# Kernel tuning notes

Hardware: AMD Instinct MI355X
Metric: run time of the kernel (lower is better)

Reference implementation:

```python
import jax, jax.numpy as jnp
import numpy as np

B, N, M, F_DIM, H, D = 4, 2048, 2048, 512, 8, 64  # M == num_time
MID = H * D
EPS = 1e-5


def _layernorm(x, w, b):
    mu = jnp.mean(x, axis=-1, keepdims=True)
    var = jnp.var(x, axis=-1, keepdims=True)
    return (x - mu) * jax.lax.rsqrt(var + EPS) * w + b


def setup_inputs() -> dict:
    key = jax.random.key(0)
    ks = jax.random.split(key, 12)
    s = 0.02
    return {
        "x": jax.random.normal(ks[0], (B, N, F_DIM), jnp.float32),
        "context": jax.random.normal(ks[1], (B, M, F_DIM), jnp.float32),
        "pos_emb": jax.random.normal(ks[2], (M, F_DIM), jnp.float32) * s,  # nn.Embedding(num_time, features)
        "ln_w": jnp.ones((F_DIM,), jnp.float32),
        "ln_b": jnp.zeros((F_DIM,), jnp.float32),
        "lnc_w": jnp.ones((F_DIM,), jnp.float32),
        "lnc_b": jnp.zeros((F_DIM,), jnp.float32),
        "Wq": jax.random.normal(ks[3], (F_DIM, MID), jnp.float32) * s,
        "Wk": jax.random.normal(ks[4], (F_DIM, MID), jnp.float32) * s,
        "Wv": jax.random.normal(ks[5], (F_DIM, MID), jnp.float32) * s,
        "Wout": jax.random.normal(ks[6], (MID, F_DIM), jnp.float32) * s,
        "bout": jnp.zeros((F_DIM,), jnp.float32),
    }


def reference(x, context, pos_emb, ln_w, ln_b, lnc_w, lnc_b, Wq, Wk, Wv, Wout, bout):
    scale = D ** (-0.5)
    keys = jnp.broadcast_to(pos_emb[None], (x.shape[0], M, F_DIM))  # [B, T, F]
    xn = _layernorm(x, ln_w, ln_b)
    kn = _layernorm(keys, ln_w, ln_b)          # same norm as x (self.norm)
    cn = _layernorm(context, lnc_w, lnc_b)
    q = (xn @ Wq).reshape(x.shape[0], N, H, D).transpose(0, 2, 1, 3)  # b h n d
    k = (kn @ Wk).reshape(x.shape[0], M, H, D).transpose(0, 2, 1, 3)  # b h m d
    v = (cn @ Wv).reshape(x.shape[0], M, H, D).transpose(0, 2, 1, 3)  # b h m d
    sim = jnp.einsum('bhnd,bhmd->bhnm', q, k) * scale
    attn = jax.nn.softmax(sim, axis=-1)
    out = jnp.einsum('bhnm,bhmd->bhnd', attn, v)
    out = out.transpose(0, 2, 1, 3).reshape(x.shape[0], N, MID)  # b n (h d)
    return out @ Wout + bout
```

## Files before the change

### kernel.cpp

```cpp
#include <hip/hip_runtime.h>
#include <stdint.h>

#define B_ 4
#define N_ 2048
#define M_ 2048
#define F_ 512
#define H_ 8
#define D_ 64

typedef __bf16 bf16x8 __attribute__((ext_vector_type(8)));
typedef float f32x4 __attribute__((ext_vector_type(4)));
typedef float f32x16 __attribute__((ext_vector_type(16)));

typedef const __attribute__((address_space(1))) uint32_t* gas_ptr;
typedef __attribute__((address_space(3))) uint32_t* las_ptr;

__device__ inline ushort f32_bf16(float f) {
    union { float f; uint32_t u; } v; v.f = f;
    uint32_t r = v.u + 0x7FFFu + ((v.u >> 16) & 1u);
    return (ushort)(r >> 16);
}

__global__ __launch_bounds__(128) void prep_kernel(
    const float* __restrict__ x, const float* __restrict__ ctx, const float* __restrict__ pos,
    const float* __restrict__ lnw, const float* __restrict__ lnb,
    const float* __restrict__ lncw, const float* __restrict__ lncb,
    const float* __restrict__ Wq, const float* __restrict__ Wk,
    const float* __restrict__ Wv, const float* __restrict__ Wo,
    ushort* __restrict__ xn, ushort* __restrict__ kn, ushort* __restrict__ cn,
    ushort* __restrict__ WqT, ushort* __restrict__ WkT,
    ushort* __restrict__ WvT, ushort* __restrict__ WoT)
{
    __shared__ float red[4];
    __shared__ float tile[32][33];
    int r = blockIdx.x;
    int tid = threadIdx.x;

    if (r < B_ * N_ + M_ + B_ * M_) {
        const float* src; ushort* dst; const float* w; const float* bp;
        if (r < B_ * N_) {
            src = x + (size_t)r * F_; dst = xn + (size_t)r * F_; w = lnw; bp = lnb;
        } else if (r < B_ * N_ + M_) {
            int rr = r - B_ * N_;
            src = pos + (size_t)rr * F_; dst = kn + (size_t)rr * F_; w = lnw; bp = lnb;
        } else {
            int rr = r - (B_ * N_ + M_);
            src = ctx + (size_t)rr * F_; dst = cn + (size_t)rr * F_; w = lncw; bp = lncb;
        }
        int wave = tid >> 6, lane = tid & 63;
        float4 v = reinterpret_cast<const float4*>(src)[tid];
        float s = v.x + v.y + v.z + v.w;
        float sq = v.x * v.x + v.y * v.y + v.z * v.z + v.w * v.w;
        #pragma unroll
        for (int mask = 1; mask < 64; mask <<= 1) {
            s += __shfl_xor(s, mask, 64);
            sq += __shfl_xor(sq, mask, 64);
        }
        if (lane == 0) { red[wave * 2] = s; red[wave * 2 + 1] = sq; }
        __syncthreads();
        float S = red[0] + red[2], SQ = red[1] + red[3];
        float mean = S * (1.0f / F_);
        float var = SQ * (1.0f / F_) - mean * mean;
        float rstd = rsqrtf(var + 1e-5f);
        float4 wv = reinterpret_cast<const float4*>(w)[tid];
        float4 bv = reinterpret_cast<const float4*>(bp)[tid];
        ushort4 o;
        o.x = f32_bf16((v.x - mean) * rstd * wv.x + bv.x);
        o.y = f32_bf16((v.y - mean) * rstd * wv.y + bv.y);
        o.z = f32_bf16((v.z - mean) * rstd * wv.z + bv.z);
        o.w = f32_bf16((v.w - mean) * rstd * wv.w + bv.w);
        reinterpret_cast<ushort4*>(dst)[tid] = o;
        return;
    }

    int wblk = r - (B_ * N_ + M_ + B_ * M_);
    const float* W; ushort* WT;
    switch (wblk >> 8) {
        case 0: W = Wq; WT = WqT; break;
        case 1: W = Wk; WT = WkT; break;
        case 2: W = Wv; WT = WvT; break;
        default: W = Wo; WT = WoT; break;
    }
    int ti = wblk & 255;
    int n0 = (ti & 15) * 32, k0 = (ti >> 4) * 32;
    int tx = tid & 31, ty = tid >> 5;
    #pragma unroll
    for (int j = 0; j < 8; ++j)
        tile[ty + j * 4][tx] = W[(size_t)(k0 + ty + j * 4) * F_ + n0 + tx];
    __syncthreads();
    #pragma unroll
    for (int j = 0; j < 8; ++j)
        WT[(size_t)(n0 + ty + j * 4) * F_ + k0 + tx] = f32_bf16(tile[tx][ty + j * 4]);
}

__device__ __forceinline__ void gemm_body(
    const ushort* __restrict__ A, const ushort* __restrict__ BT,
    const float* __restrict__ bias, void* __restrict__ Cout,
    int mode, int bx, int by)
{
    __shared__ ushort As[128][64];
    __shared__ ushort Bs[128][64];
    int tid = threadIdx.x;
    int row0 = by * 128, col0 = bx * 128;
    int wv = tid >> 6, lane = tid & 63;
    int wm = wv >> 1, wn = wv & 1;
    f32x4 acc[4][4] = {};

    const int lrow8 = lane >> 3;
    const int chs = ((lane & 7) ^ (lrow8 & 7)) * 8;
    const ushort* agp = A + (size_t)(row0 + wv * 32 + lrow8) * F_ + chs;
    const ushort* bgp = BT + (size_t)(col0 + wv * 32 + lrow8) * F_ + chs;

    for (int k0 = 0; k0 < F_; k0 += 64) {
        #pragma unroll
        for (int j = 0; j < 4; ++j) {
            __builtin_amdgcn_global_load_lds(
                (gas_ptr)(const void*)(agp + k0 + j * 8 * F_),
                (las_ptr)(void*)&As[wv * 32 + j * 8][0], 16, 0, 0);
            __builtin_amdgcn_global_load_lds(
                (gas_ptr)(const void*)(bgp + k0 + j * 8 * F_),
                (las_ptr)(void*)&Bs[wv * 32 + j * 8][0], 16, 0, 0);
        }
        __syncthreads();
        #pragma unroll
        for (int kt = 0; kt < 2; ++kt) {
            int lrow = lane & 15;
            int ch = ((kt * 4 + (lane >> 4)) ^ (lane & 7)) * 8;
            bf16x8 af[4], bfr[4];
            #pragma unroll
            for (int mt = 0; mt < 4; ++mt)
                af[mt] = *reinterpret_cast<const bf16x8*>(&As[wm * 64 + mt * 16 + lrow][ch]);
            #pragma unroll
            for (int nt = 0; nt < 4; ++nt)
                bfr[nt] = *reinterpret_cast<const bf16x8*>(&Bs[wn * 64 + nt * 16 + lrow][ch]);
            #pragma unroll
            for (int mt = 0; mt < 4; ++mt)
                #pragma unroll
                for (int nt = 0; nt < 4; ++nt)
                    acc[mt][nt] = __builtin_amdgcn_mfma_f32_16x16x32_bf16(
                        af[mt], bfr[nt], acc[mt][nt], 0, 0, 0);
        }
        __syncthreads();
    }

    int lr4 = (lane >> 4) * 4, lc = lane & 15;
    #pragma unroll
    for (int mt = 0; mt < 4; ++mt) {
        #pragma unroll
        for (int nt = 0; nt < 4; ++nt) {
            int ccol = col0 + wn * 64 + nt * 16 + lc;
            float bv = (mode == 1) ? bias[ccol] : 0.0f;
            #pragma unroll
            for (int j = 0; j < 4; ++j) {
                int crow = row0 + wm * 64 + mt * 16 + lr4 + j;
                float val = acc[mt][nt][j] + bv;
                if (mode == 1) {
                    reinterpret_cast<float*>(Cout)[(size_t)crow * F_ + ccol] = val;
                } else if (mode == 0) {
                    reinterpret_cast<ushort*>(Cout)[(size_t)crow * F_ + ccol] = f32_bf16(val);
                } else if (mode == 2) {
                    int h = ccol >> 6, t = crow >> 7, s = (crow >> 6) & 1;
                    int ab = (crow >> 5) & 1, l31 = crow & 31;
                    int ds = (ccol >> 4) & 3, g2 = (ccol >> 3) & 1, e = ccol & 7;
                    size_t addr = (((size_t)(h * 16 + t) * 16 + s * 8 + ds * 2 + ab) * 64
                                   + g2 * 32 + l31) * 8 + e;
                    reinterpret_cast<ushort*>(Cout)[addr] = f32_bf16(val);
                } else {
                    int b2 = crow >> 11, m = crow & 2047;
                    int h = ccol >> 6, d = ccol & 63;
                    int bh = b2 * 8 + h, hh = d >> 5, l31 = d & 31;
                    int t = m >> 7, s = (m >> 6) & 1, s_ = (m >> 4) & 3;
                    int g2 = (m >> 3) & 1, i = m & 7;
                    size_t addr = (((size_t)(bh * 16 + t) * 16 + hh * 8 + s * 4 + s_) * 64
                                   + g2 * 32 + l31) * 8 + i;
                    reinterpret_cast<ushort*>(Cout)[addr] = f32_bf16(val);
                }
            }
        }
    }
}

__global__ __launch_bounds__(256) void qkv_gemm_kernel(
    const ushort* __restrict__ xn, const ushort* __restrict__ kn,
    const ushort* __restrict__ cn,
    const ushort* __restrict__ WqT, const ushort* __restrict__ WkT,
    const ushort* __restrict__ WvT,
    ushort* __restrict__ qb, ushort* __restrict__ kF, ushort* __restrict__ vF)
{
    int bid = blockIdx.x;
    if (bid < 256) {
        gemm_body(xn, WqT, nullptr, (void*)qb, 0, bid & 3, bid >> 2);
    } else if (bid < 320) {
        int t = bid - 256;
        gemm_body(kn, WkT, nullptr, (void*)kF, 2, t & 3, t >> 2);
    } else {
        int t = bid - 320;
        gemm_body(cn, WvT, nullptr, (void*)vF, 3, t & 3, t >> 2);
    }
}

__global__ __launch_bounds__(256) void out_gemm_kernel(
    const ushort* __restrict__ A, const ushort* __restrict__ WoT,
    const float* __restrict__ bias, float* __restrict__ out)
{
    gemm_body(A, WoT, bias, (void*)out, 1, blockIdx.x & 3, blockIdx.x >> 2);
}

#define MAKE_PA(dst, p, ss) do {                                               \
    uint32_t w0_, w1_, w2_, w3_;                                               \
    asm("v_cvt_pk_bf16_f32 %0, %1, %2" : "=v"(w0_) : "v"(p[8*(ss)+0]), "v"(p[8*(ss)+1])); \
    asm("v_cvt_pk_bf16_f32 %0, %1, %2" : "=v"(w1_) : "v"(p[8*(ss)+2]), "v"(p[8*(ss)+3])); \
    asm("v_cvt_pk_bf16_f32 %0, %1, %2" : "=v"(w2_) : "v"(p[8*(ss)+4]), "v"(p[8*(ss)+5])); \
    asm("v_cvt_pk_bf16_f32 %0, %1, %2" : "=v"(w3_) : "v"(p[8*(ss)+6]), "v"(p[8*(ss)+7])); \
    asm("v_permlane32_swap_b32 %0, %1" : "+v"(w0_), "+v"(w2_));                \
    asm("v_permlane32_swap_b32 %0, %1" : "+v"(w1_), "+v"(w3_));                \
    union { uint32_t w[4]; bf16x8 v; } u_;                                     \
    u_.w[0] = w0_; u_.w[1] = w1_; u_.w[2] = w2_; u_.w[3] = w3_;                \
    dst = u_.v;                                                                \
} while (0)

#define KLOAD(DST, u) do {                                                     \
    const ushort* _p = kfb_ + (size_t)(u) * 4096 + lane * 8;                   \
    _Pragma("unroll")                                                          \
    for (int f_ = 0; f_ < 8; ++f_)                                             \
        DST[f_] = *reinterpret_cast<const bf16x8*>(_p + f_ * 512);             \
} while (0)

#define VLOAD(DST, u) do {                                                     \
    const ushort* _p = vfb_ + (size_t)((u) >> 1) * 8192 +                      \
                       ((u) & 1) * 4 * 512 + lane * 8;                         \
    _Pragma("unroll")                                                          \
    for (int hh_ = 0; hh_ < 2; ++hh_)                                          \
        _Pragma("unroll")                                                      \
        for (int s2_ = 0; s2_ < 4; ++s2_)                                      \
            DST[hh_ * 4 + s2_] = *reinterpret_cast<const bf16x8*>(             \
                _p + (hh_ * 8 + s2_) * 512);                                   \
} while (0)

#define COMPUTE_HALF(QF, OACC, LR, AB) do {                                    \
    f32x16 sS;                                                                 \
    _Pragma("unroll")                                                          \
    for (int j = 0; j < 16; ++j) sS[j] = 0.0f;                                 \
    __builtin_amdgcn_s_setprio(1);                                             \
    _Pragma("unroll")                                                          \
    for (int ds_ = 0; ds_ < 4; ++ds_)                                          \
        sS = __builtin_amdgcn_mfma_f32_32x32x16_bf16(kR[ds_ * 2 + (AB)], QF[ds_], sS, 0, 0, 0); \
    __builtin_amdgcn_s_setprio(0);                                             \
    float pf[16];                                                              \
    _Pragma("unroll")                                                          \
    for (int j = 0; j < 16; ++j)                                               \
        pf[j] = __builtin_amdgcn_exp2f(sS[j] * c1);                            \
    float r0 = 0.0f, r1 = 0.0f, r2 = 0.0f, r3 = 0.0f;                          \
    _Pragma("unroll")                                                          \
    for (int j = 0; j < 16; j += 4) {                                          \
        r0 += pf[j];     r1 += pf[j + 1];                                      \
        r2 += pf[j + 2]; r3 += pf[j + 3];                                      \
    }                                                                          \
    LR += (r0 + r1) + (r2 + r3);                                               \
    bf16x8 pa0, pa1;                                                           \
    MAKE_PA(pa0, pf, 0);                                                       \
    MAKE_PA(pa1, pf, 1);                                                       \
    __builtin_amdgcn_s_setprio(1);                                             \
    _Pragma("unroll")                                                          \
    for (int hh = 0; hh < 2; ++hh) {                                           \
        OACC[hh] = __builtin_amdgcn_mfma_f32_32x32x16_bf16(                    \
            pa0, vR[hh * 4 + (AB) * 2], OACC[hh], 0, 0, 0);                    \
        OACC[hh] = __builtin_amdgcn_mfma_f32_32x32x16_bf16(                    \
            pa1, vR[hh * 4 + (AB) * 2 + 1], OACC[hh], 0, 0, 0);                \
    }                                                                          \
    __builtin_amdgcn_s_setprio(0);                                             \
} while (0)

__global__ __launch_bounds__(512, 1) void attn_kernel(
    const ushort* __restrict__ q,
    const ushort* __restrict__ kF,
    const ushort* __restrict__ vF,
    ushort* __restrict__ o)
{
    const int wave = threadIdx.x >> 6, lane = threadIdx.x & 63;
    const int l31 = lane & 31, g = lane >> 5;
    const int qpair = wave & 3, half = wave >> 2;
    const int bid = blockIdx.x;
    const int qx = bid >> 5, bh = bid & 31;
    const int b = bh >> 3, h = bh & 7;
    const int q0 = qx * 256 + qpair * 64;

    __shared__ float ols[4][64][64];
    __shared__ float lls[4][2][64];

    bf16x8 qfA[4], qfB[4];
    const ushort* qrowA = q + (size_t)(b * N_ + q0 + l31) * F_ + h * 64 + g * 8;
    const ushort* qrowB = qrowA + 32 * F_;
    #pragma unroll
    for (int ds = 0; ds < 4; ++ds) {
        qfA[ds] = *reinterpret_cast<const bf16x8*>(qrowA + ds * 16);
        qfB[ds] = *reinterpret_cast<const bf16x8*>(qrowB + ds * 16);
    }

    float l0 = 0.0f, l1 = 0.0f;
    f32x16 oaccA[2], oaccB[2];
    #pragma unroll
    for (int hh = 0; hh < 2; ++hh)
        #pragma unroll
        for (int j = 0; j < 16; ++j) { oaccA[hh][j] = 0.0f; oaccB[hh][j] = 0.0f; }

    const ushort* kfb_ = kF + (size_t)h * 16 * 16 * 512;
    const ushort* vfb_ = vF + (size_t)bh * 16 * 16 * 512;
    const float c1 = 0.18033688f;

    bf16x8 kR[8], vR[8];
    const int ubase = half * 16;

    #pragma unroll 1
    for (int uu = 0; uu < 16; ++uu) {
        int u = ubase + uu;
        KLOAD(kR, u);
        VLOAD(vR, u);
        COMPUTE_HALF(qfA, oaccA, l0, 0);
        COMPUTE_HALF(qfB, oaccB, l1, 0);
        COMPUTE_HALF(qfA, oaccA, l0, 1);
        COMPUTE_HALF(qfB, oaccB, l1, 1);
    }

    l0 += __shfl_xor(l0, 32, 64);
    l1 += __shfl_xor(l1, 32, 64);

    if (half) {
        #pragma unroll
        for (int hh = 0; hh < 2; ++hh)
            #pragma unroll
            for (int j = 0; j < 16; ++j) {
                ols[qpair][hh * 16 + j][lane] = oaccA[hh][j];
                ols[qpair][32 + hh * 16 + j][lane] = oaccB[hh][j];
            }
        lls[qpair][0][lane] = l0;
        lls[qpair][1][lane] = l1;
    }
    __syncthreads();
    if (!half) {
        #pragma unroll
        for (int hh = 0; hh < 2; ++hh)
            #pragma unroll
            for (int j = 0; j < 16; ++j) {
                oaccA[hh][j] += ols[qpair][hh * 16 + j][lane];
                oaccB[hh][j] += ols[qpair][32 + hh * 16 + j][lane];
            }
        l0 += lls[qpair][0][lane];
        l1 += lls[qpair][1][lane];
        float li0 = 1.0f / l0, li1 = 1.0f / l1;
        float rli0[16], rli1[16];
        #pragma unroll
        for (int j = 0; j < 16; ++j) {
            int idx = 8 * (j >> 2) + 4 * g + (j & 3);
            rli0[j] = __shfl(li0, idx, 64);
            rli1[j] = __shfl(li1, idx, 64);
        }
        #pragma unroll
        for (int hh = 0; hh < 2; ++hh)
            #pragma unroll
            for (int j = 0; j < 16; ++j) {
                int qr = (j & 3) + 8 * (j >> 2) + 4 * g;
                o[(size_t)(b * N_ + q0 + qr) * F_ + h * 64 + hh * 32 + l31] =
                    f32_bf16(oaccA[hh][j] * rli0[j]);
                o[(size_t)(b * N_ + q0 + 32 + qr) * F_ + h * 64 + hh * 32 + l31] =
                    f32_bf16(oaccB[hh][j] * rli1[j]);
            }
    }
}

extern "C" void kernel_launch(void* const* d_in, const int* in_sizes, int n_in,
                              void* d_out, int out_size, void* d_ws, size_t ws_size,
                              hipStream_t stream) {
    const float* x    = (const float*)d_in[0];
    const float* ctx  = (const float*)d_in[1];
    const float* pos  = (const float*)d_in[2];
    const float* lnw  = (const float*)d_in[3];
    const float* lnb  = (const float*)d_in[4];
    const float* lncw = (const float*)d_in[5];
    const float* lncb = (const float*)d_in[6];
    const float* Wq   = (const float*)d_in[7];
    const float* Wk   = (const float*)d_in[8];
    const float* Wv   = (const float*)d_in[9];
    const float* Wo   = (const float*)d_in[10];
    const float* bout = (const float*)d_in[11];
    float* out = (float*)d_out;

    char* ws = (char*)d_ws;
    ushort* xn  = (ushort*)(ws + 0);
    ushort* cn  = (ushort*)(ws + 8388608);
    ushort* kn  = (ushort*)(ws + 16777216);
    ushort* WqT = (ushort*)(ws + 18874368);
    ushort* WkT = (ushort*)(ws + 19398656);
    ushort* WvT = (ushort*)(ws + 19922944);
    ushort* WoT = (ushort*)(ws + 20447232);
    ushort* qb  = (ushort*)(ws + 20971520);
    ushort* kFb = (ushort*)(ws + 29360128);
    ushort* vFb = (ushort*)(ws + 39845888);
    ushort* ao  = (ushort*)(ws + 48234496);

    hipLaunchKernelGGL(prep_kernel, dim3(B_ * N_ + M_ + B_ * M_ + 1024), dim3(128),
                       0, stream,
                       x, ctx, pos, lnw, lnb, lncw, lncb, Wq, Wk, Wv, Wo,
                       xn, kn, cn, WqT, WkT, WvT, WoT);
    hipLaunchKernelGGL(qkv_gemm_kernel, dim3(576), dim3(256), 0, stream,
                       xn, kn, cn, WqT, WkT, WvT, qb, kFb, vFb);
    hipLaunchKernelGGL(attn_kernel, dim3(256), dim3(512), 0, stream,
                       qb, kFb, vFb, ao);
    hipLaunchKernelGGL(out_gemm_kernel, dim3(256), dim3(256), 0, stream,
                       ao, WoT, bout, out);
}
```

Baseline: 92.47 us.

## Split attention KV range into quarters across waves, doubling block count

Each attention block now covers 128 query rows instead of 256, and its 8 waves split the key/value sequence four ways instead of two. The grid grows from 256 to 512 blocks, and launch bounds now request two blocks per CU. This is meant to fill the GPU's CUs better and shorten each wave's serial loop. In exchange, the partial softmax sums and output accumulators must be merged through shared memory in a multi-step reduction with several extra barriers, which adds LDS traffic and sync overhead.

```diff
diff --git a/kernel.cpp b/kernel.cpp
--- a/kernel.cpp
+++ b/kernel.cpp
@@ -271,7 +271,7 @@
     __builtin_amdgcn_s_setprio(0);                                             \
 } while (0)
 
-__global__ __launch_bounds__(512, 1) void attn_kernel(
+__global__ __launch_bounds__(512, 2) void attn_kernel(
     const ushort* __restrict__ q,
     const ushort* __restrict__ kF,
     const ushort* __restrict__ vF,
@@ -279,14 +279,14 @@
 {
     const int wave = threadIdx.x >> 6, lane = threadIdx.x & 63;
     const int l31 = lane & 31, g = lane >> 5;
-    const int qpair = wave & 3, half = wave >> 2;
+    const int qslot = wave & 1, quarter = wave >> 1;
     const int bid = blockIdx.x;
     const int qx = bid >> 5, bh = bid & 31;
     const int b = bh >> 3, h = bh & 7;
-    const int q0 = qx * 256 + qpair * 64;
-
-    __shared__ float ols[4][64][64];
-    __shared__ float lls[4][2][64];
+    const int q0 = qx * 128 + qslot * 64;
+
+    __shared__ float mbuf[2][2][32][64];
+    __shared__ float lbuf[2][2][64];
 
     bf16x8 qfA[4], qfB[4];
     const ushort* qrowA = q + (size_t)(b * N_ + q0 + l31) * F_ + h * 64 + g * 8;
@@ -309,10 +309,10 @@
     const float c1 = 0.18033688f;
 
     bf16x8 kR[8], vR[8];
-    const int ubase = half * 16;
+    const int ubase = quarter * 8;
 
     #pragma unroll 1
-    for (int uu = 0; uu < 16; ++uu) {
+    for (int uu = 0; uu < 8; ++uu) {
         int u = ubase + uu;
         KLOAD(kR, u);
         VLOAD(vR, u);
@@ -325,28 +325,65 @@
     l0 += __shfl_xor(l0, 32, 64);
     l1 += __shfl_xor(l1, 32, 64);
 
-    if (half) {
+    const int slot = quarter >> 1;
+    if (quarter & 1) {
+        #pragma unroll
+        for (int hh = 0; hh < 2; ++hh)
+            #pragma unroll
+            for (int j = 0; j < 16; ++j)
+                mbuf[qslot][slot][hh * 16 + j][lane] = oaccA[hh][j];
+        lbuf[qslot][slot][lane] = l0;
+    }
+    __syncthreads();
+    if (!(quarter & 1)) {
+        #pragma unroll
+        for (int hh = 0; hh < 2; ++hh)
+            #pragma unroll
+            for (int j = 0; j < 16; ++j)
+                oaccA[hh][j] += mbuf[qslot][slot][hh * 16 + j][lane];
+        l0 += lbuf[qslot][slot][lane];
+    }
+    __syncthreads();
+    if (quarter & 1) {
+        #pragma unroll
+        for (int hh = 0; hh < 2; ++hh)
+            #pragma unroll
+            for (int j = 0; j < 16; ++j)
+                mbuf[qslot][slot][hh * 16 + j][lane] = oaccB[hh][j];
+        lbuf[qslot][slot][lane] = l1;
+    }
+    __syncthreads();
+    if (!(quarter & 1)) {
+        #pragma unroll
+        for (int hh = 0; hh < 2; ++hh)
+            #pragma unroll
+            for (int j = 0; j < 16; ++j)
+                oaccB[hh][j] += mbuf[qslot][slot][hh * 16 + j][lane];
+        l1 += lbuf[qslot][slot][lane];
+    }
+    __syncthreads();
+    if (quarter == 2) {
         #pragma unroll
         for (int hh = 0; hh < 2; ++hh)
             #pragma unroll
             for (int j = 0; j < 16; ++j) {
-                ols[qpair][hh * 16 + j][lane] = oaccA[hh][j];
-                ols[qpair][32 + hh * 16 + j][lane] = oaccB[hh][j];
+                mbuf[qslot][0][hh * 16 + j][lane] = oaccA[hh][j];
+                mbuf[qslot][1][hh * 16 + j][lane] = oaccB[hh][j];
             }
-        lls[qpair][0][lane] = l0;
-        lls[qpair][1][lane] = l1;
-    }
-    __syncthreads();
-    if (!half) {
+        lbuf[qslot][0][lane] = l0;
+        lbuf[qslot][1][lane] = l1;
+    }
+    __syncthreads();
+    if (quarter == 0) {
         #pragma unroll
         for (int hh = 0; hh < 2; ++hh)
             #pragma unroll
             for (int j = 0; j < 16; ++j) {
-                oaccA[hh][j] += ols[qpair][hh * 16 + j][lane];
-                oaccB[hh][j] += ols[qpair][32 + hh * 16 + j][lane];
+                oaccA[hh][j] += mbuf[qslot][0][hh * 16 + j][lane];
+                oaccB[hh][j] += mbuf[qslot][1][hh * 16 + j][lane];
             }
-        l0 += lls[qpair][0][lane];
-        l1 += lls[qpair][1][lane];
+        l0 += lbuf[qslot][0][lane];
+        l1 += lbuf[qslot][1][lane];
         float li0 = 1.0f / l0, li1 = 1.0f / l1;
         float rli0[16], rli1[16];
         #pragma unroll
@@ -404,7 +441,7 @@
                        xn, kn, cn, WqT, WkT, WvT, WoT);
     hipLaunchKernelGGL(qkv_gemm_kernel, dim3(576), dim3(256), 0, stream,
                        xn, kn, cn, WqT, WkT, WvT, qb, kFb, vFb);
-    hipLaunchKernelGGL(attn_kernel, dim3(256), dim3(512), 0, stream,
+    hipLaunchKernelGGL(attn_kernel, dim3(512), dim3(512), 0, stream,
                        qb, kFb, vFb, ao);
     hipLaunchKernelGGL(out_gemm_kernel, dim3(256), dim3(256), 0, stream,
                        ao, WoT, bout, out);
```

Measured after the change: 96.59 us. 1.04x slower.
